# Kernel tuning notes

Hardware: AMD Instinct MI355X
Metric: run time of the kernel (lower is better)

The kernel has to match this reference:

```python
import jax, jax.numpy as jnp
import numpy as np

B, S, D, H = 2, 2048, 1024, 16
HD = D // H

def setup_inputs() -> dict:
    key = jax.random.key(0)
    ks = jax.random.split(key, 9)
    s = 1.0 / np.sqrt(D)
    inp = {"x": jax.random.normal(ks[0], (B, S, D), dtype=jnp.float32)}
    for i, name in enumerate(["q", "k", "v", "g"]):
        inp[f"W{name}"] = jax.random.uniform(ks[1 + i], (D, D), minval=-s, maxval=s, dtype=jnp.float32)
        inp[f"b{name}"] = jax.random.uniform(ks[5 + i], (D,), minval=-s, maxval=s, dtype=jnp.float32)
    return inp

def reference(x, Wq, bq, Wk, bk, Wv, bv, Wg, bg):
    # projections: [B,S,D] -> [B,H,S,HD]
    def proj(W, b):
        y = x @ W.T + b
        return y.reshape(B, S, H, HD).transpose(0, 2, 1, 3)
    q = proj(Wq, bq)
    k = proj(Wk, bk)
    v = proj(Wv, bv)
    g = proj(Wg, bg)
    qg = jax.nn.gelu(q * g, approximate=False)  # gate + activation before scores
    att = jnp.einsum("bhqd,bhkd->bhqk", qg, k)  # note: no 1/sqrt(d) scaling in original
    att = jax.nn.softmax(att, axis=-1)
    out = jnp.einsum("bhqk,bhkd->bhqd", att, v)
    return out.transpose(0, 2, 1, 3).reshape(B, S, D)
```

## Files before the change

kernel.cpp:

```cpp
#include <hip/hip_runtime.h>
#include <hip/hip_bf16.h>
#include <stdint.h>

#define PB 2
#define PS 2048
#define PD 1024
#define PH 16
#define PHD 64
#define PM (PB*PS)

typedef _Float16 half8 __attribute__((ext_vector_type(8)));
typedef _Float16 half4v __attribute__((ext_vector_type(4)));
typedef __fp16   fp16x2 __attribute__((ext_vector_type(2)));
typedef float    f32x4 __attribute__((ext_vector_type(4)));

__device__ __forceinline__ void ld_g2l_16(const void* g, void* l) {
  __builtin_amdgcn_global_load_lds(
      (const __attribute__((address_space(1))) unsigned int*)g,
      (__attribute__((address_space(3))) unsigned int*)l, 16, 0, 0);
}

__global__ void convert_f32_f16(const float* __restrict__ src,
                                _Float16* __restrict__ dst, int n8) {
  int i = blockIdx.x * blockDim.x + threadIdx.x;
  if (i >= n8) return;
  float4 f0 = reinterpret_cast<const float4*>(src)[2*i];
  float4 f1 = reinterpret_cast<const float4*>(src)[2*i+1];
  half8 o;
  o[0]=(_Float16)f0.x; o[1]=(_Float16)f0.y; o[2]=(_Float16)f0.z; o[3]=(_Float16)f0.w;
  o[4]=(_Float16)f1.x; o[5]=(_Float16)f1.y; o[6]=(_Float16)f1.z; o[7]=(_Float16)f1.w;
  reinterpret_cast<half8*>(dst)[i] = o;
}

__global__ void convert4_f32_f16(const float* __restrict__ w0, const float* __restrict__ w1,
                                 const float* __restrict__ w2, const float* __restrict__ w3,
                                 _Float16* __restrict__ dst, int n8) {
  int i = blockIdx.x * blockDim.x + threadIdx.x;
  if (i >= n8) return;
  int z = blockIdx.y;
  const float* src = (z==0)?w0:(z==1)?w1:(z==2)?w2:w3;
  float4 f0 = reinterpret_cast<const float4*>(src)[2*i];
  float4 f1 = reinterpret_cast<const float4*>(src)[2*i+1];
  half8 o;
  o[0]=(_Float16)f0.x; o[1]=(_Float16)f0.y; o[2]=(_Float16)f0.z; o[3]=(_Float16)f0.w;
  o[4]=(_Float16)f1.x; o[5]=(_Float16)f1.y; o[6]=(_Float16)f1.z; o[7]=(_Float16)f1.w;
  reinterpret_cast<half8*>(dst + (size_t)z*1024*1024)[i] = o;
}

__global__ __launch_bounds__(256, 2) void proj_fused(
    const _Float16* __restrict__ xh, const _Float16* __restrict__ wh,
    const float* __restrict__ bqp, const float* __restrict__ bkp,
    const float* __restrict__ bvp, const float* __restrict__ bgp,
    _Float16* __restrict__ qg, _Float16* __restrict__ kf,
    _Float16* __restrict__ vT)
{
  const int K = 1024;
  __shared__ _Float16 As[2][128*32];
  __shared__ _Float16 Bs0[2][128*32];
  __shared__ _Float16 Bs1[2][128*32];
  const int z = blockIdx.z;
  const size_t w0off = (size_t)(z==0 ? 0 : 1) * (1024*1024);
  const size_t w1off = (size_t)(z==0 ? 3 : 2) * (1024*1024);
  const float* bias0 = (z==0) ? bqp : bkp;
  const float* bias1 = (z==0) ? bgp : bvp;
  const int m0 = blockIdx.x * 128;
  const int n0 = blockIdx.y * 128;
  const int t = threadIdx.x;
  const int lane = t & 63;
  const int w = t >> 6;
  const int wr = w >> 1, wc = w & 1;
  const int lm = lane & 15, quad = lane >> 4;
  const int scb = (((lane&3) ^ ((lane>>3)&3)))*8;
  const int rblk = ((quad ^ ((lm>>1)&3)))*8;

  auto stage = [&](int buf, int k0) {
    #pragma unroll
    for (int c=0;c<2;c++) {
      int lin = c*256 + t;
      int row = lin >> 2;
      size_t ga = (size_t)(m0+row)*K + k0 + scb;
      size_t gb = (size_t)(n0+row)*K + k0 + scb;
      int lo8 = (c*256 + w*64)*8;
      ld_g2l_16(&xh[ga], &As[buf][lo8]);
      ld_g2l_16(&wh[w0off + gb], &Bs0[buf][lo8]);
      ld_g2l_16(&wh[w1off + gb], &Bs1[buf][lo8]);
    }
  };

  f32x4 acc0[4][4], acc1[4][4];
  #pragma unroll
  for (int i=0;i<4;i++)
    #pragma unroll
    for (int j=0;j<4;j++) {
      acc0[i][j] = (f32x4){0.f,0.f,0.f,0.f};
      acc1[i][j] = (f32x4){0.f,0.f,0.f,0.f};
    }

  stage(0, 0);
  __syncthreads();

  for (int k0 = 0; k0 < K; k0 += 32) {
    const int cur = (k0 >> 5) & 1;
    if (k0 + 32 < K) stage(cur ^ 1, k0 + 32);

    half8 ah[4];
    #pragma unroll
    for (int i=0;i<4;i++)
      ah[i] = *reinterpret_cast<const half8*>(&As[cur][(wr*64 + i*16 + lm)*32 + rblk]);
    #pragma unroll
    for (int j=0;j<4;j++) {
      const int bo = (wc*64 + j*16 + lm)*32 + rblk;
      half8 b0 = *reinterpret_cast<const half8*>(&Bs0[cur][bo]);
      half8 b1 = *reinterpret_cast<const half8*>(&Bs1[cur][bo]);
      #pragma unroll
      for (int i=0;i<4;i++) {
        acc0[i][j] = __builtin_amdgcn_mfma_f32_16x16x32_f16(ah[i], b0, acc0[i][j], 0,0,0);
        acc1[i][j] = __builtin_amdgcn_mfma_f32_16x16x32_f16(ah[i], b1, acc1[i][j], 0,0,0);
      }
    }
    __syncthreads();
  }
  #pragma unroll
  for (int j=0;j<4;j++) {
    int n = n0 + wc*64 + j*16 + lm;
    float b0 = bias0[n];
    float b1 = bias1[n];
    #pragma unroll
    for (int i=0;i<4;i++) {
      int mb = m0 + wr*64 + i*16 + quad*4;
      #pragma unroll
      for (int r=0;r<4;r++) {
        int token = mb + r;
        float v0 = acc0[i][j][r] + b0;
        float v1 = acc1[i][j][r] + b1;
        if (z == 0) {
          float xx = v0 * v1;
          float y = 0.5f * xx * (1.0f + erff(xx * 0.70710678118f));
          qg[(size_t)token*PD + n] = (_Float16)(y * 1.44269504f);
        } else {
          kf[(size_t)token*PD + n] = (_Float16)v0;
          int bb2 = token >> 11, ss = token & 2047;
          int hh = n >> 6, dd = n & 63;
          vT[((size_t)((bb2*16 + hh)*64 + dd))*2048 + ss] = (_Float16)v1;
        }
      }
    }
  }
}

__global__ __launch_bounds__(256) void flash_attn(
    const _Float16* __restrict__ QG,
    const _Float16* __restrict__ Kp,
    const _Float16* __restrict__ VT,
    float* __restrict__ out)
{
  __shared__ _Float16 Ks[2][64*64];
  __shared__ _Float16 Vts[64*64];
  __shared__ _Float16 Pss[4][16*72];
  const int t = threadIdx.x;
  const int lane = t & 63, w = t >> 6;
  const int lm = lane & 15, quad = lane >> 4;
  const int bh = blockIdx.y;
  const int b = bh >> 4, h = bh & 15;
  const int qb = blockIdx.x * 64 + w * 16;
  const size_t kbase = (size_t)b * PS * PD + (size_t)h * PHD;
  const size_t vtb = (size_t)bh * 64 * 2048;

  const int lrow = lane >> 3;
  const int lcb  = ((lane & 7) ^ lrow) * 8;
  const int kblk0 = ((quad     ^ (lm&7)))*8;
  const int kblk1 = (((quad+4) ^ (lm&7)))*8;

  half8 qf[2];
  {
    size_t qrow = kbase + (size_t)(qb + lm) * PD;
    qf[0] = *reinterpret_cast<const half8*>(&QG[qrow + quad*8]);
    qf[1] = *reinterpret_cast<const half8*>(&QG[qrow + 32 + quad*8]);
  }

  f32x4 o[4];
  #pragma unroll
  for (int dc=0;dc<4;dc++) o[dc] = (f32x4){0.f,0.f,0.f,0.f};
  float lsum = 0.f;

  const _Float16* kgp = &Kp[kbase + (size_t)(w*8 + lrow)*PD + lcb];
  const _Float16* vgp = &VT[vtb + (size_t)(w*8 + lrow)*2048 + lcb];
  _Float16* vdst0 = &Vts[((w*8 + lrow)*8 + (lane & 7))*8];
  _Float16* vdst1 = vdst0 + 32*64;

  const f32x4 sinit = {-11.54156036f, -11.54156036f, -11.54156036f, -11.54156036f};

  ld_g2l_16(kgp,                        &Ks[0][(w*8)*64]);
  ld_g2l_16(kgp + (size_t)32*PD,        &Ks[0][(32 + w*8)*64]);
  ld_g2l_16(vgp,                        &Vts[(w*8)*64]);
  ld_g2l_16(vgp + (size_t)32*2048,      &Vts[(32 + w*8)*64]);
  __syncthreads();

  for (int kt = 0; kt < PS; kt += 64) {
    const int buf = (kt >> 6) & 1;
    const bool nx = (kt + 64) < PS;
    float4 vr0, vr1;
    if (nx) {
      ld_g2l_16(kgp + (size_t)(kt+64)*PD, &Ks[buf^1][(w*8)*64]);
      ld_g2l_16(kgp + (size_t)(kt+96)*PD, &Ks[buf^1][(32 + w*8)*64]);
      vr0 = *reinterpret_cast<const float4*>(vgp + kt + 64);
      vr1 = *reinterpret_cast<const float4*>(vgp + (size_t)32*2048 + kt + 64);
    }

    f32x4 s[4];
    __builtin_amdgcn_s_setprio(1);
    #pragma unroll
    for (int ns=0; ns<4; ns++) {
      const int rb = (ns*16 + lm)*64;
      half8 kf0 = *reinterpret_cast<const half8*>(&Ks[buf][rb + kblk0]);
      half8 kf1 = *reinterpret_cast<const half8*>(&Ks[buf][rb + kblk1]);
      f32x4 a = sinit;
      a = __builtin_amdgcn_mfma_f32_16x16x32_f16(kf0, qf[0], a, 0,0,0);
      a = __builtin_amdgcn_mfma_f32_16x16x32_f16(kf1, qf[1], a, 0,0,0);
      s[ns] = a;
    }
    __builtin_amdgcn_s_setprio(0);

    #pragma unroll
    for (int ns=0; ns<4; ns++) {
      float p0 = fminf(__builtin_amdgcn_exp2f(s[ns][0]), 60000.0f);
      float p1 = fminf(__builtin_amdgcn_exp2f(s[ns][1]), 60000.0f);
      float p2 = fminf(__builtin_amdgcn_exp2f(s[ns][2]), 60000.0f);
      float p3 = fminf(__builtin_amdgcn_exp2f(s[ns][3]), 60000.0f);
      lsum += (p0+p1) + (p2+p3);
      union { struct { fp16x2 a, b; } s2; half4v v; } u;
      u.s2.a = __builtin_amdgcn_cvt_pkrtz(p0, p1);
      u.s2.b = __builtin_amdgcn_cvt_pkrtz(p2, p3);
      *reinterpret_cast<half4v*>(&Pss[w][lm*72 + ns*16 + quad*4]) = u.v;
    }

    half8 pa0 = *reinterpret_cast<const half8*>(&Pss[w][lm*72 + quad*8]);
    half8 pa1 = *reinterpret_cast<const half8*>(&Pss[w][lm*72 + 32 + quad*8]);
    __builtin_amdgcn_s_setprio(1);
    #pragma unroll
    for (int dc=0;dc<4;dc++) {
      const int vb = (dc*16 + lm)*64;
      half8 vb0 = *reinterpret_cast<const half8*>(&Vts[vb + kblk0]);
      half8 vb1 = *reinterpret_cast<const half8*>(&Vts[vb + kblk1]);
      o[dc] = __builtin_amdgcn_mfma_f32_16x16x32_f16(pa0, vb0, o[dc], 0,0,0);
      o[dc] = __builtin_amdgcn_mfma_f32_16x16x32_f16(pa1, vb1, o[dc], 0,0,0);
    }
    __builtin_amdgcn_s_setprio(0);

    __syncthreads();
    if (nx) {
      *reinterpret_cast<float4*>(vdst0) = vr0;
      *reinterpret_cast<float4*>(vdst1) = vr1;
    }
    __syncthreads();
  }

  float l = lsum;
  l += __shfl_xor(l, 16);
  l += __shfl_xor(l, 32);
  float inv = 1.0f / l;
  #pragma unroll
  for (int r=0;r<4;r++) {
    int m = quad*4 + r;
    float invr = __shfl(inv, m);
    int row = qb + m;
    size_t ob = kbase + (size_t)row * PD;
    #pragma unroll
    for (int dc=0;dc<4;dc++) {
      out[ob + dc*16 + lm] = o[dc][r] * invr;
    }
  }
}

extern "C" void kernel_launch(void* const* d_in, const int* in_sizes, int n_in,
                              void* d_out, int out_size, void* d_ws, size_t ws_size,
                              hipStream_t stream) {
  const float* x  = (const float*)d_in[0];
  const float* Wq = (const float*)d_in[1];
  const float* bq = (const float*)d_in[2];
  const float* Wk = (const float*)d_in[3];
  const float* bk = (const float*)d_in[4];
  const float* Wv = (const float*)d_in[5];
  const float* bv = (const float*)d_in[6];
  const float* Wg = (const float*)d_in[7];
  const float* bg = (const float*)d_in[8];
  float* out = (float*)d_out;

  char* ws = (char*)d_ws;
  const size_t MB = 1u << 20;
  _Float16* xh = (_Float16*)(ws + 0*MB);
  _Float16* wh = (_Float16*)(ws + 8*MB);
  _Float16* qg = (_Float16*)(ws + 16*MB);
  _Float16* kf = (_Float16*)(ws + 24*MB);
  _Float16* vT = (_Float16*)(ws + 32*MB);

  const int NW = 1024*1024;
  const int NX = PM*PD;

  convert_f32_f16<<<NX/8/256, 256, 0, stream>>>(x, xh, NX/8);
  convert4_f32_f16<<<dim3(NW/8/256, 4), 256, 0, stream>>>(Wq, Wk, Wv, Wg, wh, NW/8);

  proj_fused<<<dim3(PM/128, PD/128, 2), 256, 0, stream>>>(
      xh, wh, bq, bk, bv, bg, qg, kf, vT);

  flash_attn<<<dim3(PS/64, PB*PH), 256, 0, stream>>>(qg, kf, vT, out);
}
```

Measured before the change: 196.7 us.

## Split fused dual-projection GEMM into four single-output GEMMs and move gating into attention

The projection kernel now computes one weight matrix per block (grid z=4) instead of two paired accumulators, halving LDS and accumulator registers so occupancy can rise to 3 blocks per CU. The q*g GELU gating moves into the flash attention prologue, which now reads separate Q and G buffers. The V transpose goes through swizzled shared memory so it can use coalesced 16-byte stores instead of scattered 2-byte writes. The two conversion kernels are merged into a single launch. The cost is an extra G buffer written and read back, and the x tile loaded twice as often across blocks.

```diff
diff --git a/kernel.cpp b/kernel.cpp
--- a/kernel.cpp
+++ b/kernel.cpp
@@ -20,49 +20,44 @@
       (__attribute__((address_space(3))) unsigned int*)l, 16, 0, 0);
 }
 
-__global__ void convert_f32_f16(const float* __restrict__ src,
-                                _Float16* __restrict__ dst, int n8) {
+__global__ void convert_all(const float* __restrict__ x,
+                            const float* __restrict__ w0, const float* __restrict__ w1,
+                            const float* __restrict__ w2, const float* __restrict__ w3,
+                            _Float16* __restrict__ xh, _Float16* __restrict__ wh) {
   int i = blockIdx.x * blockDim.x + threadIdx.x;
-  if (i >= n8) return;
-  float4 f0 = reinterpret_cast<const float4*>(src)[2*i];
-  float4 f1 = reinterpret_cast<const float4*>(src)[2*i+1];
+  const float* src;
+  _Float16* dst;
+  int idx;
+  if (blockIdx.y == 0) {
+    src = x; dst = xh; idx = i;
+  } else {
+    int wsel = i >> 17;
+    idx = i & 131071;
+    src = (wsel==0)?w0:(wsel==1)?w1:(wsel==2)?w2:w3;
+    dst = wh + (size_t)wsel * 1048576;
+  }
+  float4 f0 = reinterpret_cast<const float4*>(src)[2*idx];
+  float4 f1 = reinterpret_cast<const float4*>(src)[2*idx+1];
   half8 o;
   o[0]=(_Float16)f0.x; o[1]=(_Float16)f0.y; o[2]=(_Float16)f0.z; o[3]=(_Float16)f0.w;
   o[4]=(_Float16)f1.x; o[5]=(_Float16)f1.y; o[6]=(_Float16)f1.z; o[7]=(_Float16)f1.w;
-  reinterpret_cast<half8*>(dst)[i] = o;
-}
-
-__global__ void convert4_f32_f16(const float* __restrict__ w0, const float* __restrict__ w1,
-                                 const float* __restrict__ w2, const float* __restrict__ w3,
-                                 _Float16* __restrict__ dst, int n8) {
-  int i = blockIdx.x * blockDim.x + threadIdx.x;
-  if (i >= n8) return;
-  int z = blockIdx.y;
-  const float* src = (z==0)?w0:(z==1)?w1:(z==2)?w2:w3;
-  float4 f0 = reinterpret_cast<const float4*>(src)[2*i];
-  float4 f1 = reinterpret_cast<const float4*>(src)[2*i+1];
-  half8 o;
-  o[0]=(_Float16)f0.x; o[1]=(_Float16)f0.y; o[2]=(_Float16)f0.z; o[3]=(_Float16)f0.w;
-  o[4]=(_Float16)f1.x; o[5]=(_Float16)f1.y; o[6]=(_Float16)f1.z; o[7]=(_Float16)f1.w;
-  reinterpret_cast<half8*>(dst + (size_t)z*1024*1024)[i] = o;
-}
-
-__global__ __launch_bounds__(256, 2) void proj_fused(
+  reinterpret_cast<half8*>(dst)[idx] = o;
+}
+
+__global__ __launch_bounds__(256, 3) void proj_gemm(
     const _Float16* __restrict__ xh, const _Float16* __restrict__ wh,
-    const float* __restrict__ bqp, const float* __restrict__ bkp,
-    const float* __restrict__ bvp, const float* __restrict__ bgp,
-    _Float16* __restrict__ qg, _Float16* __restrict__ kf,
-    _Float16* __restrict__ vT)
+    const float* __restrict__ bqp, const float* __restrict__ bgp,
+    const float* __restrict__ bkp, const float* __restrict__ bvp,
+    _Float16* __restrict__ qf, _Float16* __restrict__ gf,
+    _Float16* __restrict__ kf, _Float16* __restrict__ vT)
 {
   const int K = 1024;
-  __shared__ _Float16 As[2][128*32];
-  __shared__ _Float16 Bs0[2][128*32];
-  __shared__ _Float16 Bs1[2][128*32];
+  __shared__ _Float16 Sm[16384];
   const int z = blockIdx.z;
-  const size_t w0off = (size_t)(z==0 ? 0 : 1) * (1024*1024);
-  const size_t w1off = (size_t)(z==0 ? 3 : 2) * (1024*1024);
-  const float* bias0 = (z==0) ? bqp : bkp;
-  const float* bias1 = (z==0) ? bgp : bvp;
+  const int wslot = (z==0)?0:(z==1)?3:(z==2)?1:2;
+  const size_t woff = (size_t)wslot * (1024*1024);
+  const float* bias = (z==0)?bqp:(z==1)?bgp:(z==2)?bkp:bvp;
+  _Float16* outp = (z==0)?qf:(z==1)?gf:kf;
   const int m0 = blockIdx.x * 128;
   const int n0 = blockIdx.y * 128;
   const int t = threadIdx.x;
@@ -81,20 +76,16 @@
       size_t ga = (size_t)(m0+row)*K + k0 + scb;
       size_t gb = (size_t)(n0+row)*K + k0 + scb;
       int lo8 = (c*256 + w*64)*8;
-      ld_g2l_16(&xh[ga], &As[buf][lo8]);
-      ld_g2l_16(&wh[w0off + gb], &Bs0[buf][lo8]);
-      ld_g2l_16(&wh[w1off + gb], &Bs1[buf][lo8]);
+      ld_g2l_16(&xh[ga],        &Sm[buf*4096 + lo8]);
+      ld_g2l_16(&wh[woff + gb], &Sm[8192 + buf*4096 + lo8]);
     }
   };
 
-  f32x4 acc0[4][4], acc1[4][4];
+  f32x4 acc[4][4];
   #pragma unroll
   for (int i=0;i<4;i++)
     #pragma unroll
-    for (int j=0;j<4;j++) {
-      acc0[i][j] = (f32x4){0.f,0.f,0.f,0.f};
-      acc1[i][j] = (f32x4){0.f,0.f,0.f,0.f};
-    }
+    for (int j=0;j<4;j++) acc[i][j] = (f32x4){0.f,0.f,0.f,0.f};
 
   stage(0, 0);
   __syncthreads();
@@ -106,50 +97,62 @@
     half8 ah[4];
     #pragma unroll
     for (int i=0;i<4;i++)
-      ah[i] = *reinterpret_cast<const half8*>(&As[cur][(wr*64 + i*16 + lm)*32 + rblk]);
+      ah[i] = *reinterpret_cast<const half8*>(&Sm[cur*4096 + (wr*64 + i*16 + lm)*32 + rblk]);
     #pragma unroll
     for (int j=0;j<4;j++) {
-      const int bo = (wc*64 + j*16 + lm)*32 + rblk;
-      half8 b0 = *reinterpret_cast<const half8*>(&Bs0[cur][bo]);
-      half8 b1 = *reinterpret_cast<const half8*>(&Bs1[cur][bo]);
+      half8 b = *reinterpret_cast<const half8*>(&Sm[8192 + cur*4096 + (wc*64 + j*16 + lm)*32 + rblk]);
+      #pragma unroll
+      for (int i=0;i<4;i++)
+        acc[i][j] = __builtin_amdgcn_mfma_f32_16x16x32_f16(ah[i], b, acc[i][j], 0,0,0);
+    }
+    __syncthreads();
+  }
+
+  if (z < 3) {
+    #pragma unroll
+    for (int j=0;j<4;j++) {
+      int n = n0 + wc*64 + j*16 + lm;
+      float bn = bias[n];
       #pragma unroll
       for (int i=0;i<4;i++) {
-        acc0[i][j] = __builtin_amdgcn_mfma_f32_16x16x32_f16(ah[i], b0, acc0[i][j], 0,0,0);
-        acc1[i][j] = __builtin_amdgcn_mfma_f32_16x16x32_f16(ah[i], b1, acc1[i][j], 0,0,0);
+        int mb = m0 + wr*64 + i*16 + quad*4;
+        #pragma unroll
+        for (int r=0;r<4;r++)
+          outp[(size_t)(mb+r)*PD + n] = (_Float16)(acc[i][j][r] + bn);
       }
     }
+  } else {
+    #pragma unroll
+    for (int j=0;j<4;j++) {
+      int nl = wc*64 + j*16 + lm;
+      float bn = bias[n0 + nl];
+      #pragma unroll
+      for (int i=0;i<4;i++) {
+        int tb = wr*64 + i*16 + quad*4;
+        half4v pv;
+        #pragma unroll
+        for (int r=0;r<4;r++) pv[r] = (_Float16)(acc[i][j][r] + bn);
+        int sw = (tb >> 3) ^ (nl & 15);
+        *reinterpret_cast<half4v*>(&Sm[nl*128 + sw*8 + (tb & 7)]) = pv;
+      }
+    }
     __syncthreads();
-  }
-  #pragma unroll
-  for (int j=0;j<4;j++) {
-    int n = n0 + wc*64 + j*16 + lm;
-    float b0 = bias0[n];
-    float b1 = bias1[n];
-    #pragma unroll
-    for (int i=0;i<4;i++) {
-      int mb = m0 + wr*64 + i*16 + quad*4;
-      #pragma unroll
-      for (int r=0;r<4;r++) {
-        int token = mb + r;
-        float v0 = acc0[i][j][r] + b0;
-        float v1 = acc1[i][j][r] + b1;
-        if (z == 0) {
-          float xx = v0 * v1;
-          float y = 0.5f * xx * (1.0f + erff(xx * 0.70710678118f));
-          qg[(size_t)token*PD + n] = (_Float16)(y * 1.44269504f);
-        } else {
-          kf[(size_t)token*PD + n] = (_Float16)v0;
-          int bb2 = token >> 11, ss = token & 2047;
-          int hh = n >> 6, dd = n & 63;
-          vT[((size_t)((bb2*16 + hh)*64 + dd))*2048 + ss] = (_Float16)v1;
-        }
-      }
+    const int nl2 = t >> 1, co = (t & 1) * 8;
+    const int hh = (n0 + nl2) >> 6, dd = (n0 + nl2) & 63;
+    const int bb2 = m0 >> 11;
+    const size_t vbase = ((size_t)((bb2*16 + hh)*64 + dd))*2048 + (m0 & 2047);
+    #pragma unroll
+    for (int c=0;c<8;c++) {
+      int cc = co + c;
+      half8 vv = *reinterpret_cast<const half8*>(&Sm[nl2*128 + ((cc ^ (nl2&15))<<3)]);
+      *reinterpret_cast<half8*>(&vT[vbase + cc*8]) = vv;
     }
   }
 }
 
 __global__ __launch_bounds__(256) void flash_attn(
-    const _Float16* __restrict__ QG,
+    const _Float16* __restrict__ Qf,
+    const _Float16* __restrict__ Gf,
     const _Float16* __restrict__ Kp,
     const _Float16* __restrict__ VT,
     float* __restrict__ out)
@@ -171,11 +174,22 @@
   const int kblk0 = ((quad     ^ (lm&7)))*8;
   const int kblk1 = (((quad+4) ^ (lm&7)))*8;
 
-  half8 qf[2];
+  half8 qgf[2];
   {
     size_t qrow = kbase + (size_t)(qb + lm) * PD;
-    qf[0] = *reinterpret_cast<const half8*>(&QG[qrow + quad*8]);
-    qf[1] = *reinterpret_cast<const half8*>(&QG[qrow + 32 + quad*8]);
+    half8 q0 = *reinterpret_cast<const half8*>(&Qf[qrow + quad*8]);
+    half8 q1 = *reinterpret_cast<const half8*>(&Qf[qrow + 32 + quad*8]);
+    half8 g0 = *reinterpret_cast<const half8*>(&Gf[qrow + quad*8]);
+    half8 g1 = *reinterpret_cast<const half8*>(&Gf[qrow + 32 + quad*8]);
+    #pragma unroll
+    for (int e=0;e<8;e++) {
+      float x0 = (float)q0[e] * (float)g0[e];
+      float x1 = (float)q1[e] * (float)g1[e];
+      float y0 = 0.5f * x0 * (1.0f + erff(x0 * 0.70710678118f));
+      float y1 = 0.5f * x1 * (1.0f + erff(x1 * 0.70710678118f));
+      qgf[0][e] = (_Float16)(y0 * 1.44269504f);
+      qgf[1][e] = (_Float16)(y1 * 1.44269504f);
+    }
   }
 
   f32x4 o[4];
@@ -215,8 +229,8 @@
       half8 kf0 = *reinterpret_cast<const half8*>(&Ks[buf][rb + kblk0]);
       half8 kf1 = *reinterpret_cast<const half8*>(&Ks[buf][rb + kblk1]);
       f32x4 a = sinit;
-      a = __builtin_amdgcn_mfma_f32_16x16x32_f16(kf0, qf[0], a, 0,0,0);
-      a = __builtin_amdgcn_mfma_f32_16x16x32_f16(kf1, qf[1], a, 0,0,0);
+      a = __builtin_amdgcn_mfma_f32_16x16x32_f16(kf0, qgf[0], a, 0,0,0);
+      a = __builtin_amdgcn_mfma_f32_16x16x32_f16(kf1, qgf[1], a, 0,0,0);
       s[ns] = a;
     }
     __builtin_amdgcn_s_setprio(0);
@@ -290,18 +304,15 @@
   const size_t MB = 1u << 20;
   _Float16* xh = (_Float16*)(ws + 0*MB);
   _Float16* wh = (_Float16*)(ws + 8*MB);
-  _Float16* qg = (_Float16*)(ws + 16*MB);
-  _Float16* kf = (_Float16*)(ws + 24*MB);
-  _Float16* vT = (_Float16*)(ws + 32*MB);
-
-  const int NW = 1024*1024;
-  const int NX = PM*PD;
-
-  convert_f32_f16<<<NX/8/256, 256, 0, stream>>>(x, xh, NX/8);
-  convert4_f32_f16<<<dim3(NW/8/256, 4), 256, 0, stream>>>(Wq, Wk, Wv, Wg, wh, NW/8);
-
-  proj_fused<<<dim3(PM/128, PD/128, 2), 256, 0, stream>>>(
-      xh, wh, bq, bk, bv, bg, qg, kf, vT);
-
-  flash_attn<<<dim3(PS/64, PB*PH), 256, 0, stream>>>(qg, kf, vT, out);
-}
+  _Float16* qf = (_Float16*)(ws + 16*MB);
+  _Float16* gf = (_Float16*)(ws + 24*MB);
+  _Float16* kf = (_Float16*)(ws + 32*MB);
+  _Float16* vT = (_Float16*)(ws + 40*MB);
+
+  convert_all<<<dim3(2048, 2), 256, 0, stream>>>(x, Wq, Wk, Wv, Wg, xh, wh);
+
+  proj_gemm<<<dim3(PM/128, PD/128, 4), 256, 0, stream>>>(
+      xh, wh, bq, bg, bk, bv, qf, gf, kf, vT);
+
+  flash_attn<<<dim3(PS/64, PB*PH), 256, 0, stream>>>(qf, gf, kf, vT, out);
+}
```

Result: no change. 194.8 us (-1.0%).
